# Optimization experiments

Hardware: AMD Instinct MI355X
Metric: run time of the kernel (lower is better)

## Reference

```python
import jax, jax.numpy as jnp
import numpy as np

K = 4  # hard-coded in ParticleNet.__init__

# (fan_in, fan_out) for all linear layers
_DIMS = [(10, 32), (32, 64),        # edgeconv1 MLP (2*5 -> 32 -> 64)
         (128, 96), (96, 128),      # edgeconv2 MLP (2*64 -> 96 -> 128)
         (256, 192), (192, 256),    # edgeconv3 MLP (2*128 -> 192 -> 256)
         (453, 453), (453, 226), (226, 2)]  # output head (5+64+128+256=453)
_PNAMES = ['c1w1', 'c1w2', 'c2w1', 'c2w2', 'c3w1', 'c3w2', 'ow1', 'ow2', 'ow3']


def setup_inputs() -> dict:
    key = jax.random.key(0)
    ks = jax.random.split(key, 2 + len(_DIMS))
    inp = {
        'coords': jax.random.normal(ks[0], (1024, 128, 2), dtype=jnp.float32),
        'features': jax.random.normal(ks[1], (1024, 128, 5), dtype=jnp.float32),
    }
    for i, (name, (fi, fo)) in enumerate(zip(_PNAMES, _DIMS)):
        inp[name] = jax.random.normal(ks[2 + i], (fi, fo), dtype=jnp.float32) / np.sqrt(fi)
        inp[name.replace('w', 'b')] = jnp.zeros((fo,), dtype=jnp.float32)
    return inp


def _knn_idx(x, k):
    # x: [B,N,C] -> idx of k nearest neighbors (excluding self): [B,N,k]
    x2 = jnp.sum(x * x, axis=-1)                              # [B,N]
    d = x2[:, :, None] + x2[:, None, :] - 2.0 * jnp.einsum('bnc,bmc->bnm', x, x)
    d = d + jnp.eye(x.shape[1], dtype=x.dtype) * 1e9          # no self-loops
    _, idx = jax.lax.top_k(-d, k)
    return idx


def _edgeconv(x, idx, w1, b1, w2, b2):
    # EdgeConv: message = MLP([x_i, x_j - x_i]), mean-aggregated over k neighbors
    xj = jax.vmap(lambda xb, ib: xb[ib])(x, idx)              # [B,N,k,C]
    xi = jnp.broadcast_to(x[:, :, None, :], xj.shape)
    h = jnp.concatenate([xi, xj - xi], axis=-1)               # [B,N,k,2C]
    h = jax.nn.elu(h @ w1 + b1)
    h = jax.nn.elu(h @ w2 + b2)
    return jnp.mean(h, axis=2)                                # [B,N,out]


def reference(coords, features, c1w1, c1b1, c1w2, c1b2, c2w1, c2b1, c2w2, c2b2,
              c3w1, c3b1, c3w2, c3b2, ow1, ob1, ow2, ob2, ow3, ob3):
    idx1 = _knn_idx(coords, K)
    out1 = _edgeconv(features, idx1, c1w1, c1b1, c1w2, c1b2)  # [B,N,64]
    idx2 = _knn_idx(out1, K)
    out2 = _edgeconv(out1, idx2, c2w1, c2b1, c2w2, c2b2)      # [B,N,128]
    idx3 = _knn_idx(out2, K)
    out3 = _edgeconv(out2, idx3, c3w1, c3b1, c3w2, c3b2)      # [B,N,256]
    h = jnp.concatenate([features, out1, out2, out3], axis=-1)  # [B,N,453]
    h = jax.nn.elu(h @ ow1 + ob1)
    h = jax.nn.elu(h @ ow2 + ob2)
    return h @ ow3 + ob3                                      # [B,N,2]
```

## Files before the change

kernel.cpp:

```cpp
#include <hip/hip_runtime.h>
#include <cstdint>
#include <cstddef>


#define NB 1024
#define NPT 128

typedef __attribute__((ext_vector_type(8))) short short8;
typedef __attribute__((ext_vector_type(4))) float floatx4;
typedef __attribute__((ext_vector_type(4))) unsigned int uint4v;

__device__ __forceinline__ float elu_f(float x) { return x > 0.0f ? x : expm1f(x); }

__device__ __forceinline__ unsigned short f2bf(float f) {
  unsigned u = __builtin_bit_cast(unsigned, f);
  unsigned r = u + 0x7FFFu + ((u >> 16) & 1u);
  return (unsigned short)(r >> 16);
}
__device__ __forceinline__ float bf2f(unsigned short h) {
  unsigned u = ((unsigned)h) << 16;
  return __builtin_bit_cast(float, u);
}

#define INS6(dv, jv)                                                    \
  if ((dv) < bd5) {                                                     \
    bd5 = (dv); bi5 = (jv);                                             \
    if (bd5 < bd4) {                                                    \
      float _t = bd4; bd4 = bd5; bd5 = _t; int _i = bi4; bi4 = bi5; bi5 = _i; \
      if (bd4 < bd3) {                                                  \
        _t = bd3; bd3 = bd4; bd4 = _t; _i = bi3; bi3 = bi4; bi4 = _i;   \
        if (bd3 < bd2) {                                                \
          _t = bd2; bd2 = bd3; bd3 = _t; _i = bi2; bi2 = bi3; bi3 = _i; \
          if (bd2 < bd1) {                                              \
            _t = bd1; bd1 = bd2; bd2 = _t; _i = bi1; bi1 = bi2; bi2 = _i; \
            if (bd1 < bd0) {                                            \
              _t = bd0; bd0 = bd1; bd1 = _t; _i = bi0; bi0 = bi1; bi1 = _i; \
            } } } } } }

template<int C>
__global__ __launch_bounds__(128) void knn_kernel(const float* __restrict__ x,
                                                  int* __restrict__ idx) {
  __shared__ __align__(16) float xs[NPT][C + 4];
  __shared__ float x2s[NPT];
  __shared__ double x2d[NPT];
  const int b = blockIdx.x, t = threadIdx.x;
  const float* xb = x + (size_t)b * NPT * C;
  for (int e = t; e < NPT * C; e += 128) xs[e / C][e % C] = xb[e];
  __syncthreads();
  float xi[C];
  float s2 = 0.0f;
  double s2d = 0.0;
#pragma unroll
  for (int c = 0; c < C; ++c) {
    xi[c] = xs[t][c];
    s2 += xi[c] * xi[c];
    s2d += (double)xi[c] * (double)xi[c];
  }
  x2s[t] = s2;
  x2d[t] = s2d;
  __syncthreads();
  float bd0 = 1e30f, bd1 = 1e30f, bd2 = 1e30f, bd3 = 1e30f, bd4 = 1e30f, bd5 = 1e30f;
  int bi0 = 0, bi1 = 0, bi2 = 0, bi3 = 0, bi4 = 0, bi5 = 0;
  for (int j = 0; j < NPT; ++j) {
    if (j == t) continue;
    float dot = 0.0f;
#pragma unroll
    for (int c = 0; c < C; ++c) dot += xi[c] * xs[j][c];
    float d = s2 + x2s[j] - 2.0f * dot;
    INS6(d, j)
  }
  auto refine = [&](int j) -> double {
    double dot = 0.0;
#pragma unroll
    for (int c = 0; c < C; ++c) dot += (double)xi[c] * (double)xs[j][c];
    return s2d + x2d[j] - 2.0 * dot;
  };
  double e0 = refine(bi0), e1 = refine(bi1), e2 = refine(bi2);
  double e3 = refine(bi3), e4 = refine(bi4), e5 = refine(bi5);
#define CSWP(da, ia, db, ib)                                            \
  if ((da > db) || (da == db && ia > ib)) {                             \
    double _td = da; da = db; db = _td; int _ti = ia; ia = ib; ib = _ti; }
  CSWP(e0, bi0, e1, bi1) CSWP(e1, bi1, e2, bi2) CSWP(e2, bi2, e3, bi3)
  CSWP(e3, bi3, e4, bi4) CSWP(e4, bi4, e5, bi5)
  CSWP(e0, bi0, e1, bi1) CSWP(e1, bi1, e2, bi2) CSWP(e2, bi2, e3, bi3)
  CSWP(e3, bi3, e4, bi4)
  CSWP(e0, bi0, e1, bi1) CSWP(e1, bi1, e2, bi2) CSWP(e2, bi2, e3, bi3)
  CSWP(e0, bi0, e1, bi1) CSWP(e1, bi1, e2, bi2)
  CSWP(e0, bi0, e1, bi1)
#undef CSWP
  int* ib = idx + ((size_t)b * NPT + t) * 4;
  ib[0] = bi0; ib[1] = bi1; ib[2] = bi2; ib[3] = bi3;
}

template<int C>
__global__ __launch_bounds__(512) void knn_mfma_kernel(const float* __restrict__ x,
                                                       int* __restrict__ idx) {
  constexpr int KC = C / 32;
  constexpr int HS = C + 8;
  constexpr int FS = C + 4;
  constexpr int CQ = C / 4;
  __shared__ __align__(16) unsigned short lbuf[2 * NPT * HS];
  __shared__ float x2s[NPT];
  __shared__ double x2d[NPT];
  unsigned short* Xhi = lbuf;
  unsigned short* Xlo = lbuf + NPT * HS;
  float* Xs = reinterpret_cast<float*>(lbuf);
  const int b = blockIdx.x, t = threadIdx.x;
  const float* xb = x + (size_t)b * NPT * C;
  for (int e = t; e < NPT * C; e += 512) {
    int r = e / C, c = e % C;
    float v = xb[e];
    unsigned short h = f2bf(v);
    Xhi[r * HS + c] = h;
    Xlo[r * HS + c] = f2bf(v - bf2f(h));
  }
  {
    const int p = t >> 2, q = t & 3;
    const float4* r4 = reinterpret_cast<const float4*>(xb + p * C + q * CQ);
    float s2 = 0.f;
    double s2d = 0.0;
#pragma unroll
    for (int c4 = 0; c4 < CQ / 4; ++c4) {
      float4 v = r4[c4];
      s2 += v.x * v.x + v.y * v.y + v.z * v.z + v.w * v.w;
      s2d += (double)v.x * v.x + (double)v.y * v.y +
             (double)v.z * v.z + (double)v.w * v.w;
    }
    s2 += __shfl_xor(s2, 1);  s2 += __shfl_xor(s2, 2);
    s2d += __shfl_xor(s2d, 1); s2d += __shfl_xor(s2d, 2);
    if (q == 0) { x2s[p] = s2; x2d[p] = s2d; }
  }
  __syncthreads();
  const int w = t >> 6, l = t & 63;
  const int lr = l & 15, lq = l >> 4;
  const int iq = w * 16 + lr;
  short8 Bhi[KC], Blo[KC];
#pragma unroll
  for (int kk = 0; kk < KC; ++kk) {
    Bhi[kk] = *reinterpret_cast<const short8*>(&Xhi[iq * HS + kk * 32 + lq * 8]);
    Blo[kk] = *reinterpret_cast<const short8*>(&Xlo[iq * HS + kk * 32 + lq * 8]);
  }
  const float x2i = x2s[iq];
  float bd0 = 1e30f, bd1 = 1e30f, bd2 = 1e30f, bd3 = 1e30f, bd4 = 1e30f, bd5 = 1e30f;
  int bi0 = 0, bi1 = 0, bi2 = 0, bi3 = 0, bi4 = 0, bi5 = 0;
#pragma unroll
  for (int jt = 0; jt < 8; ++jt) {
    short8 Ahi[KC], Alo[KC];
#pragma unroll
    for (int kk = 0; kk < KC; ++kk) {
      Ahi[kk] = *reinterpret_cast<const short8*>(
          &Xhi[(jt * 16 + lr) * HS + kk * 32 + lq * 8]);
      Alo[kk] = *reinterpret_cast<const short8*>(
          &Xlo[(jt * 16 + lr) * HS + kk * 32 + lq * 8]);
    }
    floatx4 g = {0.f, 0.f, 0.f, 0.f};
#pragma unroll
    for (int kk = 0; kk < KC; ++kk) {
      g = __builtin_amdgcn_mfma_f32_16x16x32_bf16(Ahi[kk], Bhi[kk], g, 0, 0, 0);
      g = __builtin_amdgcn_mfma_f32_16x16x32_bf16(Ahi[kk], Blo[kk], g, 0, 0, 0);
      g = __builtin_amdgcn_mfma_f32_16x16x32_bf16(Alo[kk], Bhi[kk], g, 0, 0, 0);
    }
#pragma unroll
    for (int r = 0; r < 4; ++r) {
      int j = jt * 16 + lq * 4 + r;
      float d = (j == iq) ? 1e30f : (x2i + x2s[j] - 2.0f * g[r]);
      INS6(d, j)
    }
  }
#pragma unroll
  for (int rnd = 0; rnd < 2; ++rnd) {
    const int m = 16 << rnd;
    float od0 = __shfl_xor(bd0, m), od1 = __shfl_xor(bd1, m), od2 = __shfl_xor(bd2, m);
    float od3 = __shfl_xor(bd3, m), od4 = __shfl_xor(bd4, m), od5 = __shfl_xor(bd5, m);
    int oi0 = __shfl_xor(bi0, m), oi1 = __shfl_xor(bi1, m), oi2 = __shfl_xor(bi2, m);
    int oi3 = __shfl_xor(bi3, m), oi4 = __shfl_xor(bi4, m), oi5 = __shfl_xor(bi5, m);
    INS6(od0, oi0) INS6(od1, oi1) INS6(od2, oi2)
    INS6(od3, oi3) INS6(od4, oi4) INS6(od5, oi5)
  }
  bi0 = __shfl(bi0, lr); bi1 = __shfl(bi1, lr); bi2 = __shfl(bi2, lr);
  bi3 = __shfl(bi3, lr); bi4 = __shfl(bi4, lr); bi5 = __shfl(bi5, lr);
  __syncthreads();
  for (int e = t; e < NPT * C; e += 512) {
    int r = e / C, c = e % C;
    Xs[r * FS + c] = xb[e];
  }
  __syncthreads();
  const double x2di = x2d[iq];
  auto refine = [&](int j) -> double {
    double dot = 0.0;
    const float* ri = &Xs[iq * FS + lq * CQ];
    const float* rj = &Xs[j * FS + lq * CQ];
#pragma unroll
    for (int c = 0; c < CQ; ++c) dot += (double)ri[c] * (double)rj[c];
    dot += __shfl_xor(dot, 16);
    dot += __shfl_xor(dot, 32);
    return x2di + x2d[j] - 2.0 * dot;
  };
  double e0 = refine(bi0), e1 = refine(bi1), e2 = refine(bi2);
  double e3 = refine(bi3), e4 = refine(bi4), e5 = refine(bi5);
#define CSWP(da, ia, db, ib)                                            \
  if ((da > db) || (da == db && ia > ib)) {                             \
    double _td = da; da = db; db = _td; int _ti = ia; ia = ib; ib = _ti; }
  CSWP(e0, bi0, e1, bi1) CSWP(e1, bi1, e2, bi2) CSWP(e2, bi2, e3, bi3)
  CSWP(e3, bi3, e4, bi4) CSWP(e4, bi4, e5, bi5)
  CSWP(e0, bi0, e1, bi1) CSWP(e1, bi1, e2, bi2) CSWP(e2, bi2, e3, bi3)
  CSWP(e3, bi3, e4, bi4)
  CSWP(e0, bi0, e1, bi1) CSWP(e1, bi1, e2, bi2) CSWP(e2, bi2, e3, bi3)
  CSWP(e0, bi0, e1, bi1) CSWP(e1, bi1, e2, bi2)
  CSWP(e0, bi0, e1, bi1)
#undef CSWP
  if (lq == 0) {
    int* ib = idx + ((size_t)b * NPT + iq) * 4;
    ib[0] = bi0; ib[1] = bi1; ib[2] = bi2; ib[3] = bi3;
  }
}

__global__ __launch_bounds__(256) void ec1_kernel(
    const float* __restrict__ feat, const int* __restrict__ idx,
    const float* __restrict__ w1, const float* __restrict__ b1,
    const float* __restrict__ w2, const float* __restrict__ b2,
    float* __restrict__ out) {
  __shared__ __align__(16) float fs[NPT][6];
  __shared__ __align__(16) float w1s[10][32];
  __shared__ __align__(16) float w2s[32][68];
  __shared__ float hs[256][33];
  __shared__ float b1s[32], b2s[64];
  const int z = blockIdx.x, t = threadIdx.x;
  const int b = z >> 1, hh = z & 1;
  const float* fb = feat + (size_t)b * NPT * 5;
  for (int e = t; e < NPT * 5; e += 256) fs[e / 5][e % 5] = fb[e];
  for (int e = t; e < 320; e += 256) w1s[e / 32][e % 32] = w1[e];
  for (int e = t; e < 2048; e += 256) w2s[e >> 6][e & 63] = w2[e];
  if (t < 32) b1s[t] = b1[t];
  if (t >= 192) b2s[t - 192] = b2[t - 192];
  __syncthreads();
  {
    const int p = hh * 64 + (t >> 2);
    const int j = idx[(size_t)b * 512 + p * 4 + (t & 3)];
    float h[32];
#pragma unroll
    for (int o = 0; o < 32; ++o) h[o] = b1s[o];
#pragma unroll
    for (int c = 0; c < 10; ++c) {
      float in_c = (c < 5) ? fs[p][c] : (fs[j][c - 5] - fs[p][c - 5]);
      const float4* wr = reinterpret_cast<const float4*>(&w1s[c][0]);
#pragma unroll
      for (int o4 = 0; o4 < 8; ++o4) {
        float4 w = wr[o4];
        h[4 * o4 + 0] += in_c * w.x; h[4 * o4 + 1] += in_c * w.y;
        h[4 * o4 + 2] += in_c * w.z; h[4 * o4 + 3] += in_c * w.w;
      }
    }
#pragma unroll
    for (int o = 0; o < 32; ++o) hs[t][o] = elu_f(h[o]);
  }
  __syncthreads();
  {
    const int g = t >> 2, q = t & 3;
    const int o0 = q * 16;
    float acc[4][16];
#pragma unroll
    for (int m = 0; m < 16; ++m) {
      float bv = b2s[o0 + m];
#pragma unroll
      for (int i = 0; i < 4; ++i) acc[i][m] = bv;
    }
    for (int k = 0; k < 32; ++k) {
      float hk0 = hs[g * 4 + 0][k];
      float hk1 = hs[g * 4 + 1][k];
      float hk2 = hs[g * 4 + 2][k];
      float hk3 = hs[g * 4 + 3][k];
      const float4* wr = reinterpret_cast<const float4*>(&w2s[k][o0]);
#pragma unroll
      for (int m4 = 0; m4 < 4; ++m4) {
        float4 w = wr[m4];
        acc[0][4 * m4 + 0] += hk0 * w.x; acc[0][4 * m4 + 1] += hk0 * w.y;
        acc[0][4 * m4 + 2] += hk0 * w.z; acc[0][4 * m4 + 3] += hk0 * w.w;
        acc[1][4 * m4 + 0] += hk1 * w.x; acc[1][4 * m4 + 1] += hk1 * w.y;
        acc[1][4 * m4 + 2] += hk1 * w.z; acc[1][4 * m4 + 3] += hk1 * w.w;
        acc[2][4 * m4 + 0] += hk2 * w.x; acc[2][4 * m4 + 1] += hk2 * w.y;
        acc[2][4 * m4 + 2] += hk2 * w.z; acc[2][4 * m4 + 3] += hk2 * w.w;
        acc[3][4 * m4 + 0] += hk3 * w.x; acc[3][4 * m4 + 1] += hk3 * w.y;
        acc[3][4 * m4 + 2] += hk3 * w.z; acc[3][4 * m4 + 3] += hk3 * w.w;
      }
    }
    float* ob = out + ((size_t)b * NPT + hh * 64 + g) * 64 + o0;
#pragma unroll
    for (int m4 = 0; m4 < 4; ++m4) {
      float4 v;
      float* vp = &v.x;
#pragma unroll
      for (int s = 0; s < 4; ++s) {
        int m = 4 * m4 + s;
        vp[s] = 0.25f * (elu_f(acc[0][m]) + elu_f(acc[1][m]) +
                         elu_f(acc[2][m]) + elu_f(acc[3][m]));
      }
      *reinterpret_cast<float4*>(&ob[4 * m4]) = v;
    }
  }
}

__global__ __launch_bounds__(512, 2) void ec2a_kernel(
    const float* __restrict__ x, const int* __restrict__ idx,
    const float* __restrict__ w1, const float* __restrict__ b1,
    float* __restrict__ H) {
  __shared__ __align__(16) float xs[NPT][68];
  __shared__ __align__(16) float w1s[128][100];
  __shared__ float b1s[96];
  const int b = blockIdx.x, t = threadIdx.x;
  const float* xb = x + (size_t)b * NPT * 64;
  for (int e = t; e < NPT * 64; e += 512) xs[e >> 6][e & 63] = xb[e];
  for (int e = t; e < 128 * 96; e += 512) w1s[e / 96][e % 96] = w1[e];
  if (t < 96) b1s[t] = b1[t];
  __syncthreads();
  const int pb = t >> 2, part = t & 3;
  const int n0 = part * 24;
  int jn[4];
#pragma unroll
  for (int i = 0; i < 4; ++i) jn[i] = idx[(size_t)b * 512 + pb * 4 + i];
  float acc[4][24];
#pragma unroll
  for (int m = 0; m < 24; ++m) {
    float bv = b1s[n0 + m];
#pragma unroll
    for (int i = 0; i < 4; ++i) acc[i][m] = bv;
  }
  for (int c = 0; c < 64; ++c) {
    float in_c = xs[pb][c];
    const float4* wr = reinterpret_cast<const float4*>(&w1s[c][n0]);
#pragma unroll
    for (int q4 = 0; q4 < 6; ++q4) {
      float4 wv = wr[q4];
#pragma unroll
      for (int i = 0; i < 4; ++i) {
        acc[i][4 * q4 + 0] += in_c * wv.x;
        acc[i][4 * q4 + 1] += in_c * wv.y;
        acc[i][4 * q4 + 2] += in_c * wv.z;
        acc[i][4 * q4 + 3] += in_c * wv.w;
      }
    }
  }
  for (int c = 0; c < 64; ++c) {
    float xic = xs[pb][c];
    float in0 = xs[jn[0]][c] - xic;
    float in1 = xs[jn[1]][c] - xic;
    float in2 = xs[jn[2]][c] - xic;
    float in3 = xs[jn[3]][c] - xic;
    const float4* wr = reinterpret_cast<const float4*>(&w1s[64 + c][n0]);
#pragma unroll
    for (int q4 = 0; q4 < 6; ++q4) {
      float4 wv = wr[q4];
      acc[0][4 * q4 + 0] += in0 * wv.x; acc[0][4 * q4 + 1] += in0 * wv.y;
      acc[0][4 * q4 + 2] += in0 * wv.z; acc[0][4 * q4 + 3] += in0 * wv.w;
      acc[1][4 * q4 + 0] += in1 * wv.x; acc[1][4 * q4 + 1] += in1 * wv.y;
      acc[1][4 * q4 + 2] += in1 * wv.z; acc[1][4 * q4 + 3] += in1 * wv.w;
      acc[2][4 * q4 + 0] += in2 * wv.x; acc[2][4 * q4 + 1] += in2 * wv.y;
      acc[2][4 * q4 + 2] += in2 * wv.z; acc[2][4 * q4 + 3] += in2 * wv.w;
      acc[3][4 * q4 + 0] += in3 * wv.x; acc[3][4 * q4 + 1] += in3 * wv.y;
      acc[3][4 * q4 + 2] += in3 * wv.z; acc[3][4 * q4 + 3] += in3 * wv.w;
    }
  }
#pragma unroll
  for (int i = 0; i < 4; ++i) {
    float* hrow = H + ((size_t)b * 512 + pb * 4 + i) * 96 + n0;
#pragma unroll
    for (int q4 = 0; q4 < 6; ++q4) {
      float4 v = {elu_f(acc[i][4 * q4 + 0]), elu_f(acc[i][4 * q4 + 1]),
                  elu_f(acc[i][4 * q4 + 2]), elu_f(acc[i][4 * q4 + 3])};
      *reinterpret_cast<float4*>(&hrow[4 * q4]) = v;
    }
  }
}

__global__ __launch_bounds__(512, 2) void ec2b_kernel(
    const float* __restrict__ H, const float* __restrict__ w2,
    const float* __restrict__ b2, float* __restrict__ out) {
  __shared__ __align__(16) float hsT[96][260];
  __shared__ float w2s[96][132];
  __shared__ float b2s[128];
  const int z = blockIdx.x, t = threadIdx.x;
  const int bc = z >> 1, hh = z & 1;
  const float* Hb = H + ((size_t)bc * 512 + hh * 256) * 96;
  for (int i = t; i < 256 * 96; i += 512) hsT[i % 96][i / 96] = Hb[i];
  for (int i = t; i < 96 * 128; i += 512) w2s[i >> 7][i & 127] = w2[i];
  if (t < 128) b2s[t] = b2[t];
  __syncthreads();
  const int g = t >> 3, oq = t & 7;
  float acc[4][16];
#pragma unroll
  for (int m = 0; m < 16; ++m) {
    float bv = b2s[oq + 8 * m];
#pragma unroll
    for (int i = 0; i < 4; ++i) acc[i][m] = bv;
  }
  for (int k = 0; k < 96; ++k) {
    float4 hv = *reinterpret_cast<const float4*>(&hsT[k][4 * g]);
#pragma unroll
    for (int m = 0; m < 16; ++m) {
      float wv = w2s[k][oq + 8 * m];
      acc[0][m] += hv.x * wv;
      acc[1][m] += hv.y * wv;
      acc[2][m] += hv.z * wv;
      acc[3][m] += hv.w * wv;
    }
  }
  float* orow = out + ((size_t)bc * NPT + hh * 64 + g) * 128;
#pragma unroll
  for (int m = 0; m < 16; ++m) {
    float s = elu_f(acc[0][m]) + elu_f(acc[1][m]) +
              elu_f(acc[2][m]) + elu_f(acc[3][m]);
    orow[oq + 8 * m] = 0.25f * s;
  }
}

__global__ __launch_bounds__(512, 2) void ec3a_kernel(
    const float* __restrict__ x, const int* __restrict__ idx,
    const unsigned short* __restrict__ w1t3g, const float* __restrict__ b1,
    unsigned short* __restrict__ h1) {
  __shared__ unsigned short Xb[128][136];
  __shared__ __align__(16) unsigned short W1t[192][264];
  __shared__ float b1s[192];
  __shared__ unsigned short stg[8][16][40];
  const int b = blockIdx.x, t = threadIdx.x;
  const float* xb = x + (size_t)b * NPT * 128;
  for (int e = t; e < NPT * 128; e += 512) Xb[e >> 7][e & 127] = f2bf(xb[e]);
  {
    const uint4v* src = reinterpret_cast<const uint4v*>(w1t3g);
    uint4v* dst = reinterpret_cast<uint4v*>(&W1t[0][0]);
    for (int i = t; i < 192 * 264 / 8; i += 512) dst[i] = src[i];
  }
  if (t < 192) b1s[t] = b1[t];
  __syncthreads();
  const int w = t >> 6, l = t & 63;
  const int lr = l & 15, lq = l >> 4;
  for (int mt = 0; mt < 4; ++mt) {
    const int m = (w * 4 + mt) * 16;
    const int e = m + lr;
    const int p = e >> 2;
    const int jp = idx[(size_t)b * 512 + e];
    short8 A[8];
#pragma unroll
    for (int kk = 0; kk < 4; ++kk) {
      int k0 = kk * 32 + lq * 8;
      A[kk] = *reinterpret_cast<const short8*>(&Xb[p][k0]);
    }
#pragma unroll
    for (int kk = 0; kk < 4; ++kk) {
      int k0 = kk * 32 + lq * 8;
      short8 aj = *reinterpret_cast<const short8*>(&Xb[jp][k0]);
      short8 ai = *reinterpret_cast<const short8*>(&Xb[p][k0]);
      short8 d;
#pragma unroll
      for (int q = 0; q < 8; ++q)
        d[q] = (short)f2bf(bf2f((unsigned short)aj[q]) - bf2f((unsigned short)ai[q]));
      A[4 + kk] = d;
    }
    floatx4 acc[12];
#pragma unroll
    for (int n = 0; n < 12; ++n) acc[n] = (floatx4){0.f, 0.f, 0.f, 0.f};
#pragma unroll
    for (int n = 0; n < 12; ++n) {
#pragma unroll
      for (int kk = 0; kk < 8; ++kk) {
        short8 Bf = *reinterpret_cast<const short8*>(&W1t[n * 16 + lr][kk * 32 + lq * 8]);
        acc[n] = __builtin_amdgcn_mfma_f32_16x16x32_bf16(A[kk], Bf, acc[n], 0, 0, 0);
      }
    }
#pragma unroll
    for (int pr = 0; pr < 6; ++pr) {
      float bv0 = b1s[pr * 32 + lr];
      float bv1 = b1s[pr * 32 + 16 + lr];
#pragma unroll
      for (int i = 0; i < 4; ++i) {
        stg[w][lq * 4 + i][lr]      = f2bf(elu_f(acc[2 * pr][i] + bv0));
        stg[w][lq * 4 + i][16 + lr] = f2bf(elu_f(acc[2 * pr + 1][i] + bv1));
      }
      asm volatile("s_waitcnt lgkmcnt(0)" ::: "memory");
      const unsigned short* src = &stg[w][l >> 2][(l & 3) * 8];
      uint4v vv = *reinterpret_cast<const uint4v*>(src);
      size_t dst = ((size_t)b * 512 + m + (l >> 2)) * 192 + pr * 32 + (l & 3) * 8;
      *reinterpret_cast<uint4v*>(&h1[dst]) = vv;
      asm volatile("s_waitcnt lgkmcnt(0)" ::: "memory");
    }
  }
}

__global__ __launch_bounds__(512, 2) void ec3b_kernel(
    const unsigned short* __restrict__ h1,
    const unsigned short* __restrict__ w2t3g, const float* __restrict__ b2,
    unsigned short* __restrict__ out3) {
  __shared__ __align__(16) unsigned short W2t[256][200];
  __shared__ float b2s[256];
  const int b = blockIdx.x, t = threadIdx.x;
  {
    const uint4v* src = reinterpret_cast<const uint4v*>(w2t3g);
    uint4v* dst = reinterpret_cast<uint4v*>(&W2t[0][0]);
    for (int i = t; i < 256 * 200 / 8; i += 512) dst[i] = src[i];
  }
  if (t < 256) b2s[t] = b2[t];
  __syncthreads();
  const int w = t >> 6, l = t & 63;
  const int lr = l & 15, lq = l >> 4;
  for (int mt = 0; mt < 4; ++mt) {
    const int m = (w * 4 + mt) * 16;
    floatx4 acc[16];
#pragma unroll
    for (int n = 0; n < 16; ++n) acc[n] = (floatx4){0.f, 0.f, 0.f, 0.f};
    const unsigned short* arow = h1 + ((size_t)b * 512 + m + lr) * 192;
#pragma unroll
    for (int kk = 0; kk < 6; ++kk) {
      short8 Af = *reinterpret_cast<const short8*>(&arow[kk * 32 + lq * 8]);
#pragma unroll
      for (int n = 0; n < 16; ++n) {
        short8 Bf = *reinterpret_cast<const short8*>(&W2t[n * 16 + lr][kk * 32 + lq * 8]);
        acc[n] = __builtin_amdgcn_mfma_f32_16x16x32_bf16(Af, Bf, acc[n], 0, 0, 0);
      }
    }
    unsigned short* orow = out3 + ((size_t)b * NPT + (m >> 2) + lq) * 256;
#pragma unroll
    for (int n = 0; n < 16; ++n) {
      float bv = b2s[n * 16 + lr];
      float s = 0.f;
#pragma unroll
      for (int i = 0; i < 4; ++i) s += elu_f(acc[n][i] + bv);
      orow[n * 16 + lr] = f2bf(0.25f * s);
    }
  }
}

__global__ __launch_bounds__(256) void prep_kernel(
    const float* __restrict__ hw1, const float* __restrict__ hw2,
    const float* __restrict__ c3w1, const float* __restrict__ c3w2,
    unsigned short* __restrict__ w1p, unsigned short* __restrict__ w2p,
    unsigned short* __restrict__ w1t3g, unsigned short* __restrict__ w2t3g) {
  int i = blockIdx.x * 256 + threadIdx.x;
  if (i < 512 * 480) {
    int n = i / 480, kp = i % 480;
    int ko = (kp < 5) ? kp : kp - 3;
    bool ok = ((kp < 5) || (kp >= 8 && kp < 456)) && (n < 453);
    w1p[i] = ok ? f2bf(hw1[(size_t)ko * 453 + n]) : (unsigned short)0;
  } else if (i < 512 * 480 + 256 * 480) {
    int j = i - 512 * 480;
    int n = j / 480, kp = j % 480;
    bool ok = (kp < 453) && (n < 226);
    w2p[j] = ok ? f2bf(hw2[(size_t)kp * 226 + n]) : (unsigned short)0;
  } else if (i < 512 * 480 + 256 * 480 + 192 * 264) {
    int m = i - (512 * 480 + 256 * 480);
    int n = m / 264, k = m % 264;
    w1t3g[m] = (k < 256) ? f2bf(c3w1[(size_t)k * 192 + n]) : (unsigned short)0;
  } else {
    int m = i - (512 * 480 + 256 * 480 + 192 * 264);
    if (m < 256 * 200) {
      int n = m / 200, k = m % 200;
      w2t3g[m] = (k < 192) ? f2bf(c3w2[(size_t)k * 256 + n]) : (unsigned short)0;
    }
  }
}

#define HSTR 488
#define TPSS 72
__global__ __launch_bounds__(256, 2) void head_mfma_kernel(
    const float* __restrict__ feat, const float* __restrict__ o1,
    const float* __restrict__ o2, const unsigned short* __restrict__ o3,
    const unsigned short* __restrict__ w1p, const float* __restrict__ b1,
    const unsigned short* __restrict__ w2p, const float* __restrict__ b2,
    const float* __restrict__ w3, const float* __restrict__ b3,
    float* __restrict__ out) {
  __shared__ unsigned short uA[64 * HSTR];
  __shared__ __align__(16) unsigned short tps[4][16][TPSS];
  __shared__ float b1s[512], b2s[256], w3s[512];
  const int t = threadIdx.x;
  const size_t base = (size_t)blockIdx.x * 64;

  for (int i = t; i < 512; i += 256) b1s[i] = (i < 453) ? b1[i] : 0.f;
  if (t < 256) b2s[t] = (t < 226) ? b2[t] : 0.f;
  for (int i = t; i < 512; i += 256) w3s[i] = (i < 452) ? w3[i] : 0.f;

  const int w = t >> 6, l = t & 63;
  const int lr = l & 15, lq = l >> 4;
  const int tr = t >> 2, tc = t & 3;
  const size_t grow = base + w * 16 + lr;

  short8 Af[15];
#pragma unroll
  for (int kk = 0; kk < 15; ++kk) {
    const int kbase = kk * 32 + lq * 8;
    short8 r;
    if (kbase >= 456) {
#pragma unroll
      for (int q = 0; q < 8; ++q) r[q] = 0;
    } else if (kbase >= 200) {
      r = *reinterpret_cast<const short8*>(&o3[grow * 256 + (kbase - 200)]);
    } else if (kbase >= 72) {
      const float* s = &o2[grow * 128 + (kbase - 72)];
#pragma unroll
      for (int q = 0; q < 8; ++q) r[q] = (short)f2bf(s[q]);
    } else if (kbase >= 8) {
      const float* s = &o1[grow * 64 + (kbase - 8)];
#pragma unroll
      for (int q = 0; q < 8; ++q) r[q] = (short)f2bf(s[q]);
    } else {
      const float* s = &feat[grow * 5];
#pragma unroll
      for (int q = 0; q < 8; ++q) r[q] = (q < 5) ? (short)f2bf(s[q]) : (short)0;
    }
    Af[kk] = r;
  }

  uint4v v[15];
#define WLOAD(SRC, CH)                                                   \
  {                                                                      \
    _Pragma("unroll")                                                    \
    for (int i = 0; i < 15; ++i)                                         \
      v[i] = *reinterpret_cast<const uint4v*>(                           \
          &SRC[((size_t)((CH) * 64 + tr)) * 480 + (tc + 4 * i) * 8]);    \
  }
#define WWRITE()                                                         \
  {                                                                      \
    _Pragma("unroll")                                                    \
    for (int i = 0; i < 15; ++i)                                         \
      *reinterpret_cast<uint4v*>(&uA[tr * HSTR + (tc + 4 * i) * 8]) = v[i]; \
  }

  WLOAD(w1p, 0)
  WWRITE()
  __syncthreads();

  short8 Af2[15];
#pragma unroll
  for (int ch = 0; ch < 8; ++ch) {
    if (ch < 7) WLOAD(w1p, ch + 1)
    else       WLOAD(w2p, 0)
    floatx4 a0 = {0.f, 0.f, 0.f, 0.f}, a1 = {0.f, 0.f, 0.f, 0.f};
    floatx4 a2 = {0.f, 0.f, 0.f, 0.f}, a3 = {0.f, 0.f, 0.f, 0.f};
#pragma unroll
    for (int kk = 0; kk < 15; ++kk) {
      int ko = kk * 32 + lq * 8;
      short8 B0 = *reinterpret_cast<const short8*>(&uA[(lr)*HSTR + ko]);
      short8 B1 = *reinterpret_cast<const short8*>(&uA[(16 + lr) * HSTR + ko]);
      short8 B2 = *reinterpret_cast<const short8*>(&uA[(32 + lr) * HSTR + ko]);
      short8 B3 = *reinterpret_cast<const short8*>(&uA[(48 + lr) * HSTR + ko]);
      a0 = __builtin_amdgcn_mfma_f32_16x16x32_bf16(Af[kk], B0, a0, 0, 0, 0);
      a1 = __builtin_amdgcn_mfma_f32_16x16x32_bf16(Af[kk], B1, a1, 0, 0, 0);
      a2 = __builtin_amdgcn_mfma_f32_16x16x32_bf16(Af[kk], B2, a2, 0, 0, 0);
      a3 = __builtin_amdgcn_mfma_f32_16x16x32_bf16(Af[kk], B3, a3, 0, 0, 0);
    }
    {
      floatx4 aj[4] = {a0, a1, a2, a3};
#pragma unroll
      for (int jx = 0; jx < 4; ++jx) {
        int c = ch * 64 + jx * 16 + lr;
        float bb = b1s[c];
#pragma unroll
        for (int i = 0; i < 4; ++i)
          tps[w][lq * 4 + i][jx * 16 + lr] = f2bf(elu_f(aj[jx][i] + bb));
      }
    }
    asm volatile("s_waitcnt lgkmcnt(0)" ::: "memory");
    Af2[2 * ch] = *reinterpret_cast<const short8*>(&tps[w][lr][lq * 8]);
    if (ch < 7)
      Af2[2 * ch + 1] = *reinterpret_cast<const short8*>(&tps[w][lr][32 + lq * 8]);
    asm volatile("s_waitcnt lgkmcnt(0)" ::: "memory");
    __syncthreads();
    WWRITE()
    __syncthreads();
  }

  float p0[4] = {0.f, 0.f, 0.f, 0.f}, p1[4] = {0.f, 0.f, 0.f, 0.f};
#pragma unroll
  for (int ch = 0; ch < 4; ++ch) {
    if (ch < 3) WLOAD(w2p, ch + 1)
    floatx4 a0 = {0.f, 0.f, 0.f, 0.f}, a1 = {0.f, 0.f, 0.f, 0.f};
    floatx4 a2 = {0.f, 0.f, 0.f, 0.f}, a3 = {0.f, 0.f, 0.f, 0.f};
#pragma unroll
    for (int kk = 0; kk < 15; ++kk) {
      int ko = kk * 32 + lq * 8;
      short8 B0 = *reinterpret_cast<const short8*>(&uA[(lr)*HSTR + ko]);
      short8 B1 = *reinterpret_cast<const short8*>(&uA[(16 + lr) * HSTR + ko]);
      short8 B2 = *reinterpret_cast<const short8*>(&uA[(32 + lr) * HSTR + ko]);
      short8 B3 = *reinterpret_cast<const short8*>(&uA[(48 + lr) * HSTR + ko]);
      a0 = __builtin_amdgcn_mfma_f32_16x16x32_bf16(Af2[kk], B0, a0, 0, 0, 0);
      a1 = __builtin_amdgcn_mfma_f32_16x16x32_bf16(Af2[kk], B1, a1, 0, 0, 0);
      a2 = __builtin_amdgcn_mfma_f32_16x16x32_bf16(Af2[kk], B2, a2, 0, 0, 0);
      a3 = __builtin_amdgcn_mfma_f32_16x16x32_bf16(Af2[kk], B3, a3, 0, 0, 0);
    }
    {
      floatx4 aj[4] = {a0, a1, a2, a3};
#pragma unroll
      for (int jx = 0; jx < 4; ++jx) {
        int c = ch * 64 + jx * 16 + lr;
        float bb = b2s[c];
        float wa = w3s[2 * c], wb = w3s[2 * c + 1];
#pragma unroll
        for (int i = 0; i < 4; ++i) {
          float h = (c < 226) ? elu_f(aj[jx][i] + bb) : 0.f;
          p0[i] += h * wa;
          p1[i] += h * wb;
        }
      }
    }
    if (ch < 3) {
      __syncthreads();
      WWRITE()
      __syncthreads();
    }
  }

#pragma unroll
  for (int i = 0; i < 4; ++i) {
    float a = p0[i], bvv = p1[i];
#pragma unroll
    for (int m = 1; m < 16; m <<= 1) {
      a += __shfl_xor(a, m);
      bvv += __shfl_xor(bvv, m);
    }
    if (lr == 0) {
      size_t row = base + w * 16 + lq * 4 + i;
      float2 vv = {a + b3[0], bvv + b3[1]};
      *reinterpret_cast<float2*>(&out[row * 2]) = vv;
    }
  }
#undef WLOAD
#undef WWRITE
}

extern "C" void kernel_launch(void* const* d_in, const int* in_sizes, int n_in,
                              void* d_out, int out_size, void* d_ws, size_t ws_size,
                              hipStream_t stream) {
  const float* coords = (const float*)d_in[0];
  const float* feat   = (const float*)d_in[1];
  const float* c1w1 = (const float*)d_in[2];  const float* c1b1 = (const float*)d_in[3];
  const float* c1w2 = (const float*)d_in[4];  const float* c1b2 = (const float*)d_in[5];
  const float* c2w1 = (const float*)d_in[6];  const float* c2b1 = (const float*)d_in[7];
  const float* c2w2 = (const float*)d_in[8];  const float* c2b2 = (const float*)d_in[9];
  const float* c3w1 = (const float*)d_in[10]; const float* c3b1 = (const float*)d_in[11];
  const float* c3w2 = (const float*)d_in[12]; const float* c3b2 = (const float*)d_in[13];
  const float* ow1  = (const float*)d_in[14]; const float* ob1  = (const float*)d_in[15];
  const float* ow2  = (const float*)d_in[16]; const float* ob2  = (const float*)d_in[17];
  const float* ow3  = (const float*)d_in[18]; const float* ob3  = (const float*)d_in[19];
  float* out = (float*)d_out;

  char* ws = (char*)d_ws;
  float* out1 = (float*)(ws);
  float* out2 = (float*)(ws + (32ull << 20));
  unsigned short* out3b = (unsigned short*)(ws + (96ull << 20));
  float* Hbuf2 = (float*)(ws + (96ull << 20));
  unsigned short* h1 = (unsigned short*)(ws + (162ull << 20));
  unsigned short* w1p = (unsigned short*)(ws + (212ull << 20));
  unsigned short* w2p = (unsigned short*)(ws + (212ull << 20) + (512ull << 10));
  unsigned short* w1t3g = (unsigned short*)(ws + (213ull << 20));
  unsigned short* w2t3g = (unsigned short*)(ws + (213ull << 20) + (256ull << 10));
  int* idx = (int*)(ws + (214ull << 20));

  prep_kernel<<<1838, 256, 0, stream>>>(ow1, ow2, c3w1, c3w2,
                                        w1p, w2p, w1t3g, w2t3g);
  knn_kernel<2><<<NB, 128, 0, stream>>>(coords, idx);
  ec1_kernel<<<2 * NB, 256, 0, stream>>>(feat, idx, c1w1, c1b1, c1w2, c1b2, out1);
  knn_mfma_kernel<64><<<NB, 512, 0, stream>>>(out1, idx);
  for (int c = 0; c < 2; ++c) {
    ec2a_kernel<<<512, 512, 0, stream>>>(out1 + (size_t)c * 512 * NPT * 64,
                                         idx + (size_t)c * 512 * 512,
                                         c2w1, c2b1, Hbuf2);
    ec2b_kernel<<<1024, 512, 0, stream>>>(Hbuf2, c2w2, c2b2,
                                          out2 + (size_t)c * 512 * NPT * 128);
  }
  knn_mfma_kernel<128><<<NB, 512, 0, stream>>>(out2, idx);
  for (int c = 0; c < 4; ++c) {
    ec3a_kernel<<<256, 512, 0, stream>>>(out2 + (size_t)c * 256 * NPT * 128,
                                         idx + (size_t)c * 256 * 512,
                                         w1t3g, c3b1, h1);
    ec3b_kernel<<<256, 512, 0, stream>>>(h1, w2t3g, c3b2,
                                         out3b + (size_t)c * 256 * NPT * 256);
  }
  head_mfma_kernel<<<2048, 256, 0, stream>>>(feat, out1, out2, out3b,
                                             w1p, ob1, w2p, ob2, ow3, ob3, out);
}
```

Baseline: 1.729 ms.

## Move edgeconv2 second layer to bf16x3 split MFMA and raise MFMA priority in head

Replaces the scalar FP32 FMA GEMM in ec2b with MFMA bf16 matrix ops. Both activations and weights are split into three bf16 parts (hi/mid/lo), and six cross-product MFMAs are accumulated to keep near-fp32 accuracy. The weight splits are precomputed in prep_kernel. The head kernel's MFMA loops are also wrapped in s_setprio(1)/s_setprio(0) to favour matrix issue. The activation splitting adds VALU work per element and reads H directly from global memory without staging it through LDS.

```diff
diff --git a/kernel.cpp b/kernel.cpp
--- a/kernel.cpp
+++ b/kernel.cpp
@@ -20,6 +20,14 @@
 __device__ __forceinline__ float bf2f(unsigned short h) {
   unsigned u = ((unsigned)h) << 16;
   return __builtin_bit_cast(float, u);
+}
+__device__ __forceinline__ void split3(float v, unsigned short& h,
+                                       unsigned short& m, unsigned short& l) {
+  h = f2bf(v);
+  float r = v - bf2f(h);
+  m = f2bf(r);
+  float r2 = r - bf2f(m);
+  l = f2bf(r2);
 }
 
 #define INS6(dv, jv)                                                    \
@@ -372,44 +380,56 @@
   }
 }
 
-__global__ __launch_bounds__(512, 2) void ec2b_kernel(
-    const float* __restrict__ H, const float* __restrict__ w2,
+__global__ __launch_bounds__(512) void ec2b_mfma_kernel(
+    const float* __restrict__ H, const unsigned short* __restrict__ w2s3,
     const float* __restrict__ b2, float* __restrict__ out) {
-  __shared__ __align__(16) float hsT[96][260];
-  __shared__ float w2s[96][132];
+  __shared__ __align__(16) unsigned short W[3 * 128 * 104];
   __shared__ float b2s[128];
   const int z = blockIdx.x, t = threadIdx.x;
-  const int bc = z >> 1, hh = z & 1;
-  const float* Hb = H + ((size_t)bc * 512 + hh * 256) * 96;
-  for (int i = t; i < 256 * 96; i += 512) hsT[i % 96][i / 96] = Hb[i];
-  for (int i = t; i < 96 * 128; i += 512) w2s[i >> 7][i & 127] = w2[i];
+  {
+    const uint4v* src = reinterpret_cast<const uint4v*>(w2s3);
+    uint4v* dst = reinterpret_cast<uint4v*>(W);
+    for (int i = t; i < 3 * 128 * 104 / 8; i += 512) dst[i] = src[i];
+  }
   if (t < 128) b2s[t] = b2[t];
   __syncthreads();
-  const int g = t >> 3, oq = t & 7;
-  float acc[4][16];
-#pragma unroll
-  for (int m = 0; m < 16; ++m) {
-    float bv = b2s[oq + 8 * m];
-#pragma unroll
-    for (int i = 0; i < 4; ++i) acc[i][m] = bv;
-  }
-  for (int k = 0; k < 96; ++k) {
-    float4 hv = *reinterpret_cast<const float4*>(&hsT[k][4 * g]);
-#pragma unroll
-    for (int m = 0; m < 16; ++m) {
-      float wv = w2s[k][oq + 8 * m];
-      acc[0][m] += hv.x * wv;
-      acc[1][m] += hv.y * wv;
-      acc[2][m] += hv.z * wv;
-      acc[3][m] += hv.w * wv;
-    }
-  }
-  float* orow = out + ((size_t)bc * NPT + hh * 64 + g) * 128;
-#pragma unroll
-  for (int m = 0; m < 16; ++m) {
-    float s = elu_f(acc[0][m]) + elu_f(acc[1][m]) +
-              elu_f(acc[2][m]) + elu_f(acc[3][m]);
-    orow[oq + 8 * m] = 0.25f * s;
+  const int w = t >> 6, l = t & 63;
+  const int lr = l & 15, lq = l >> 4;
+  for (int mt = 0; mt < 2; ++mt) {
+    const int m = (w * 2 + mt) * 16;
+    const size_t row = (size_t)z * 256 + m + lr;
+    short8 Ah[3], Am[3], Al[3];
+#pragma unroll
+    for (int kk = 0; kk < 3; ++kk) {
+      const float* s = &H[row * 96 + kk * 32 + lq * 8];
+#pragma unroll
+      for (int q = 0; q < 8; ++q) {
+        unsigned short hh, mm, ll;
+        split3(s[q], hh, mm, ll);
+        Ah[kk][q] = (short)hh; Am[kk][q] = (short)mm; Al[kk][q] = (short)ll;
+      }
+    }
+#pragma unroll
+    for (int nt = 0; nt < 8; ++nt) {
+      floatx4 acc = {0.f, 0.f, 0.f, 0.f};
+#pragma unroll
+      for (int kk = 0; kk < 3; ++kk) {
+        const int off = (nt * 16 + lr) * 104 + kk * 32 + lq * 8;
+        short8 Bh = *reinterpret_cast<const short8*>(&W[off]);
+        short8 Bm = *reinterpret_cast<const short8*>(&W[128 * 104 + off]);
+        short8 Bl = *reinterpret_cast<const short8*>(&W[2 * 128 * 104 + off]);
+        acc = __builtin_amdgcn_mfma_f32_16x16x32_bf16(Ah[kk], Bh, acc, 0, 0, 0);
+        acc = __builtin_amdgcn_mfma_f32_16x16x32_bf16(Ah[kk], Bm, acc, 0, 0, 0);
+        acc = __builtin_amdgcn_mfma_f32_16x16x32_bf16(Am[kk], Bh, acc, 0, 0, 0);
+        acc = __builtin_amdgcn_mfma_f32_16x16x32_bf16(Am[kk], Bm, acc, 0, 0, 0);
+        acc = __builtin_amdgcn_mfma_f32_16x16x32_bf16(Ah[kk], Bl, acc, 0, 0, 0);
+        acc = __builtin_amdgcn_mfma_f32_16x16x32_bf16(Al[kk], Bh, acc, 0, 0, 0);
+      }
+      const float bv = b2s[nt * 16 + lr];
+      float s = elu_f(acc[0] + bv) + elu_f(acc[1] + bv) +
+                elu_f(acc[2] + bv) + elu_f(acc[3] + bv);
+      out[((size_t)z * 64 + (m >> 2) + lq) * 128 + nt * 16 + lr] = 0.25f * s;
+    }
   }
 }
 
@@ -531,29 +551,39 @@
 __global__ __launch_bounds__(256) void prep_kernel(
     const float* __restrict__ hw1, const float* __restrict__ hw2,
     const float* __restrict__ c3w1, const float* __restrict__ c3w2,
+    const float* __restrict__ c2w2,
     unsigned short* __restrict__ w1p, unsigned short* __restrict__ w2p,
-    unsigned short* __restrict__ w1t3g, unsigned short* __restrict__ w2t3g) {
+    unsigned short* __restrict__ w1t3g, unsigned short* __restrict__ w2t3g,
+    unsigned short* __restrict__ w2e2) {
+  const int S0 = 512 * 480, S1 = S0 + 256 * 480, S2 = S1 + 192 * 264;
+  const int S3 = S2 + 256 * 200, S4 = S3 + 3 * 128 * 104;
   int i = blockIdx.x * 256 + threadIdx.x;
-  if (i < 512 * 480) {
+  if (i < S0) {
     int n = i / 480, kp = i % 480;
     int ko = (kp < 5) ? kp : kp - 3;
     bool ok = ((kp < 5) || (kp >= 8 && kp < 456)) && (n < 453);
     w1p[i] = ok ? f2bf(hw1[(size_t)ko * 453 + n]) : (unsigned short)0;
-  } else if (i < 512 * 480 + 256 * 480) {
-    int j = i - 512 * 480;
+  } else if (i < S1) {
+    int j = i - S0;
     int n = j / 480, kp = j % 480;
     bool ok = (kp < 453) && (n < 226);
     w2p[j] = ok ? f2bf(hw2[(size_t)kp * 226 + n]) : (unsigned short)0;
-  } else if (i < 512 * 480 + 256 * 480 + 192 * 264) {
-    int m = i - (512 * 480 + 256 * 480);
+  } else if (i < S2) {
+    int m = i - S1;
     int n = m / 264, k = m % 264;
     w1t3g[m] = (k < 256) ? f2bf(c3w1[(size_t)k * 192 + n]) : (unsigned short)0;
-  } else {
-    int m = i - (512 * 480 + 256 * 480 + 192 * 264);
-    if (m < 256 * 200) {
-      int n = m / 200, k = m % 200;
-      w2t3g[m] = (k < 192) ? f2bf(c3w2[(size_t)k * 256 + n]) : (unsigned short)0;
-    }
+  } else if (i < S3) {
+    int m = i - S2;
+    int n = m / 200, k = m % 200;
+    w2t3g[m] = (k < 192) ? f2bf(c3w2[(size_t)k * 256 + n]) : (unsigned short)0;
+  } else if (i < S4) {
+    int m = i - S3;
+    int s = m / (128 * 104), rem = m % (128 * 104);
+    int n = rem / 104, k = rem % 104;
+    float v = (k < 96) ? c2w2[(size_t)k * 128 + n] : 0.f;
+    unsigned short hh, mm, ll;
+    split3(v, hh, mm, ll);
+    w2e2[m] = (s == 0) ? hh : (s == 1) ? mm : ll;
   }
 }
 
@@ -633,6 +663,7 @@
     else       WLOAD(w2p, 0)
     floatx4 a0 = {0.f, 0.f, 0.f, 0.f}, a1 = {0.f, 0.f, 0.f, 0.f};
     floatx4 a2 = {0.f, 0.f, 0.f, 0.f}, a3 = {0.f, 0.f, 0.f, 0.f};
+    __builtin_amdgcn_s_setprio(1);
 #pragma unroll
     for (int kk = 0; kk < 15; ++kk) {
       int ko = kk * 32 + lq * 8;
@@ -645,6 +676,7 @@
       a2 = __builtin_amdgcn_mfma_f32_16x16x32_bf16(Af[kk], B2, a2, 0, 0, 0);
       a3 = __builtin_amdgcn_mfma_f32_16x16x32_bf16(Af[kk], B3, a3, 0, 0, 0);
     }
+    __builtin_amdgcn_s_setprio(0);
     {
       floatx4 aj[4] = {a0, a1, a2, a3};
 #pragma unroll
@@ -672,6 +704,7 @@
     if (ch < 3) WLOAD(w2p, ch + 1)
     floatx4 a0 = {0.f, 0.f, 0.f, 0.f}, a1 = {0.f, 0.f, 0.f, 0.f};
     floatx4 a2 = {0.f, 0.f, 0.f, 0.f}, a3 = {0.f, 0.f, 0.f, 0.f};
+    __builtin_amdgcn_s_setprio(1);
 #pragma unroll
     for (int kk = 0; kk < 15; ++kk) {
       int ko = kk * 32 + lq * 8;
@@ -684,6 +717,7 @@
       a2 = __builtin_amdgcn_mfma_f32_16x16x32_bf16(Af2[kk], B2, a2, 0, 0, 0);
       a3 = __builtin_amdgcn_mfma_f32_16x16x32_bf16(Af2[kk], B3, a3, 0, 0, 0);
     }
+    __builtin_amdgcn_s_setprio(0);
     {
       floatx4 aj[4] = {a0, a1, a2, a3};
 #pragma unroll
@@ -751,9 +785,10 @@
   unsigned short* w1t3g = (unsigned short*)(ws + (213ull << 20));
   unsigned short* w2t3g = (unsigned short*)(ws + (213ull << 20) + (256ull << 10));
   int* idx = (int*)(ws + (214ull << 20));
-
-  prep_kernel<<<1838, 256, 0, stream>>>(ow1, ow2, c3w1, c3w2,
-                                        w1p, w2p, w1t3g, w2t3g);
+  unsigned short* w2e2 = (unsigned short*)(ws + (216ull << 20));
+
+  prep_kernel<<<1994, 256, 0, stream>>>(ow1, ow2, c3w1, c3w2, c2w2,
+                                        w1p, w2p, w1t3g, w2t3g, w2e2);
   knn_kernel<2><<<NB, 128, 0, stream>>>(coords, idx);
   ec1_kernel<<<2 * NB, 256, 0, stream>>>(feat, idx, c1w1, c1b1, c1w2, c1b2, out1);
   knn_mfma_kernel<64><<<NB, 512, 0, stream>>>(out1, idx);
@@ -761,8 +796,8 @@
     ec2a_kernel<<<512, 512, 0, stream>>>(out1 + (size_t)c * 512 * NPT * 64,
                                          idx + (size_t)c * 512 * 512,
                                          c2w1, c2b1, Hbuf2);
-    ec2b_kernel<<<1024, 512, 0, stream>>>(Hbuf2, c2w2, c2b2,
-                                          out2 + (size_t)c * 512 * NPT * 128);
+    ec2b_mfma_kernel<<<1024, 512, 0, stream>>>(Hbuf2, w2e2, c2b2,
+                                               out2 + (size_t)c * 512 * NPT * 128);
   }
   knn_mfma_kernel<128><<<NB, 512, 0, stream>>>(out2, idx);
   for (int c = 0; c < 4; ++c) {
```

Result: no change. 1.717 ms (-0.7%).
